# Kernel optimization log

Hardware: AMD Instinct MI355X
Metric: run time of the kernel (lower is better)

Reference implementation:

```python
import jax, jax.numpy as jnp
import numpy as np
from jax import lax


def setup_inputs() -> dict:
    key = jax.random.key(0)
    ks = jax.random.split(key, 8)
    B, T, F, H = 256, 96, 32, 1024
    s = 0.05
    return {
        "initial_input": jax.random.normal(ks[0], (B, 1, F), jnp.float32),
        "hidden_h": jax.random.normal(ks[1], (B, H), jnp.float32),
        "hidden_c": jax.random.normal(ks[2], (B, H), jnp.float32),
        "targets": jax.random.normal(ks[3], (B, T, F), jnp.float32),
        "W_x": jax.random.normal(ks[4], (F, 4 * H), jnp.float32) * s,
        "W_h": jax.random.normal(ks[5], (H, 4 * H), jnp.float32) * s,
        "b": jnp.zeros((4 * H,), jnp.float32),
        "W_dense": jax.random.normal(ks[6], (H, F), jnp.float32) * s,
        "b_dense": jnp.zeros((F,), jnp.float32),
    }


def reference(initial_input, hidden_h, hidden_c, targets, W_x, W_h, b, W_dense, b_dense):
    # Inference-mode (training=False) decode: no teacher forcing, each step's
    # dense output is fed back as the next LSTM input. Keras LSTM gate order: i, f, c(g), o.
    T = targets.shape[1]

    def step(carry, _):
        h, c, x = carry  # h,c: [B,H], x: [B,F]
        z = x @ W_x + h @ W_h + b            # [B, 4H]
        i, f, g, o = jnp.split(z, 4, axis=-1)
        i = jax.nn.sigmoid(i)
        f = jax.nn.sigmoid(f)
        g = jnp.tanh(g)
        o = jax.nn.sigmoid(o)
        c_new = f * c + i * g
        h_new = o * jnp.tanh(c_new)
        y = h_new @ W_dense + b_dense        # [B, F]
        return (h_new, c_new, y), y

    x0 = initial_input[:, 0, :]              # [B, F]
    _, ys = lax.scan(step, (hidden_h, hidden_c, x0), None, length=T)
    return jnp.transpose(ys, (1, 0, 2))      # [B, T, F]
```

## Files before the change

kernel.cpp:

```cpp
#include <hip/hip_runtime.h>
#include <hip/hip_bf16.h>
#include <stdint.h>

#define B_SZ 256
#define H_SZ 1024
#define NG   4096
#define F_SZ 32
#define T_SZ 96

typedef __attribute__((ext_vector_type(8))) short short8;
typedef __attribute__((ext_vector_type(4))) float f32x4;

__device__ __forceinline__ unsigned short f2bf(float x) {
  unsigned int u = __float_as_uint(x);
  u += 0x7fffu + ((u >> 16) & 1u);
  return (unsigned short)(u >> 16);
}
__device__ __forceinline__ float sigf(float x) {
  float e = __expf(-x);
  return __builtin_amdgcn_rcpf(1.f + e);
}
__device__ __forceinline__ float tanh_fast(float x) {
  float e = __expf(-2.f * fabsf(x));
  float t = (1.f - e) * __builtin_amdgcn_rcpf(1.f + e);
  return copysignf(t, x);
}
__device__ __forceinline__ void stage16c(const void* g, void* l) {
  __builtin_amdgcn_global_load_lds(
      (const __attribute__((address_space(1))) void*)g,
      (__attribute__((address_space(3))) void*)l, 16, 0, 1 );
}
__device__ __forceinline__ short8 u4s8(uint4 v) {
  union { uint4 u; short8 s; } c; c.u = v; return c.s;
}

__global__ __launch_bounds__(256) void k_prep_w(
    const float* __restrict__ Wx, const float* __restrict__ Wh,
    const float* __restrict__ Wd,
    unsigned short* __restrict__ WeffT, unsigned short* __restrict__ WhT,
    unsigned short* __restrict__ WdT, unsigned int* __restrict__ flags)
{
  int tid = threadIdx.x;
  if (blockIdx.x == 512) {
    for (int i = 0; i < 33; ++i) flags[i * 256 + tid] = 0u;
    for (int i = 0; i < 128; ++i) {
      int idx = i * 256 + tid;
      int f = idx >> 10, k = idx & 1023;
      WdT[idx] = f2bf(Wd[k * 32 + f]);
    }
    return;
  }
  __shared__ float wx[32 * 256];
  __shared__ unsigned short resE[32 * 256];
  __shared__ unsigned short resH[32 * 256];
  int kt = blockIdx.x & 31, nt = blockIdx.x >> 5;
  int k0 = kt * 32, n0 = nt * 256;
  for (int i = 0; i < 32; ++i) {
    int lin = i * 256 + tid;
    wx[lin] = Wx[(size_t)(lin >> 8) * NG + n0 + (lin & 255)];
  }
  __syncthreads();
  for (int kr = 0; kr < 32; ++kr) {
    int k = k0 + kr;
    float v = Wh[(size_t)k * NG + n0 + tid];
    float acc = 0.f;
#pragma unroll
    for (int f = 0; f < 32; ++f) acc += Wd[k * 32 + f] * wx[f * 256 + tid];
    resH[kr * 256 + tid] = f2bf(v);
    resE[kr * 256 + tid] = f2bf(v + acc);
  }
  __syncthreads();
#pragma unroll
  for (int pass = 0; pass < 2; ++pass) {
    const unsigned short* res = pass ? resH : resE;
    unsigned short* dst = (pass ? WhT : WeffT) + (size_t)(n0 + tid) * H_SZ + k0;
    unsigned int vals[16];
#pragma unroll
    for (int p = 0; p < 16; ++p)
      vals[p] = (unsigned int)res[(2 * p) * 256 + tid] |
                ((unsigned int)res[(2 * p + 1) * 256 + tid] << 16);
#pragma unroll
    for (int qd = 0; qd < 4; ++qd) {
      uint4 v4; v4.x = vals[4*qd]; v4.y = vals[4*qd+1]; v4.z = vals[4*qd+2]; v4.w = vals[4*qd+3];
      ((uint4*)dst)[qd] = v4;
    }
  }
}

__global__ __launch_bounds__(512, 2) void k_persist(
    const unsigned short* __restrict__ WeffT,
    const unsigned short* __restrict__ WhT,
    const float* __restrict__ x0,
    const float* __restrict__ h0,
    const float* __restrict__ c0,
    const float* __restrict__ Wx,
    const float* __restrict__ bvec,
    const float* __restrict__ bd,
    const unsigned short* __restrict__ WdT,
    unsigned short* __restrict__ hbuf0,
    unsigned short* __restrict__ hbuf1,
    float* __restrict__ out,
    unsigned int* __restrict__ flags)
{
  const int b = blockIdx.x;
  const int xcd = b & 7, slot = b >> 3;
  const int m0A = xcd << 5;
  const int m0B = m0A + 16;
  const int nh = slot << 5;
  const int tid = threadIdx.x, lane = tid & 63, w = tid >> 6;
  const int g = w >> 1;
  const int nhh = (w & 1) << 4;

  __shared__ unsigned short AbA[32 * 512];
  __shared__ unsigned short AbB[32 * 512];
  __shared__ float zldsA[4][16][33];
  __shared__ float zldsB[4][16][33];
  __shared__ float ypA[16][32];
  __shared__ float ypB[16][32];

  unsigned int* xcctab = flags + 8192;
  unsigned int myxcc;
  asm volatile("s_getreg_b32 %0, hwreg(HW_REG_XCC_ID)" : "=s"(myxcc));
  myxcc &= 15u;

  float cregA, cregB;
  {
    int m = tid >> 5, cc = tid & 31;
    size_t giA = (size_t)(m0A + m) * H_SZ + nh + cc;
    size_t giB = (size_t)(m0B + m) * H_SZ + nh + cc;
    hbuf0[giA] = f2bf(h0[giA]);
    hbuf0[giB] = f2bf(h0[giB]);
    cregA = c0[giA];
    cregB = c0[giB];
  }
  __syncthreads();
  unsigned int* myflagA = flags + (((xcd << 5) | slot) << 4);
  unsigned int* myflagB = myflagA + 4096;
  if (tid == 0) {
    __hip_atomic_store(&xcctab[b], myxcc, __ATOMIC_RELAXED,
                       __HIP_MEMORY_SCOPE_AGENT);
    __hip_atomic_store(myflagA, 1u, __ATOMIC_RELEASE, __HIP_MEMORY_SCOPE_AGENT);
    __hip_atomic_store(myflagB, 1u, __ATOMIC_RELEASE, __HIP_MEMORY_SCOPE_AGENT);
  }

  const int col = lane & 15;
  const int kq = lane >> 4;
  const int n0a = (g << 10) + nh + nhh + col;
  float bfv = bvec[n0a];
  float u0rA[4], u0rB[4];
#pragma unroll
  for (int e = 0; e < 4; ++e) { u0rA[e] = bfv; u0rB[e] = bfv; }
  for (int f = 0; f < 32; ++f) {
    float wxf = Wx[(size_t)f * NG + n0a];
    bfv += bd[f] * wxf;
#pragma unroll
    for (int e = 0; e < 4; ++e) {
      int row = (kq << 2) + e;
      u0rA[e] += x0[(m0A + row) * 32 + f] * wxf;
      u0rB[e] += x0[(m0B + row) * 32 + f] * wxf;
    }
  }

  uint4 wr[32];
  {
    const unsigned short* p0 = WhT + (size_t)n0a * H_SZ + (kq << 3);
#pragma unroll
    for (int kk = 0; kk < 32; ++kk) wr[kk] = *(const uint4*)(p0 + kk * 32);
#pragma unroll
    for (int kk = 0; kk < 32; ++kk)
      asm volatile("" : "+v"(wr[kk].x), "+v"(wr[kk].y),
                        "+v"(wr[kk].z), "+v"(wr[kk].w));
  }

  const int srow = lane >> 2;
  const int skg  = (lane & 3) ^ ((lane >> 3) & 3);
  const int sgbase = srow * H_SZ + (w << 5) + (skg << 3);
  const int q = kq ^ ((col >> 1) & 3);
  const int aoff = col * 32 + (q << 3);
  const int yf = tid & 31, ykc = tid >> 5;
  const int yrow = slot & 15;
  const int ysw = (slot >> 1) & 3;
  const bool yIsA = (slot < 16);
  const unsigned short* wdp = WdT + (size_t)yf * H_SZ + ykc * 64;
  const unsigned int* pollpA = flags + (((xcd << 5) | (lane & 31)) << 4);
  const unsigned int* pollpB = pollpA + 4096;

  bool pure = false;
  for (int j = 0; j <= T_SZ; ++j) {
    const unsigned int tgt = (unsigned)(j + 1);
    while (true) {
      unsigned int v = __hip_atomic_load(pollpA, __ATOMIC_RELAXED,
                                         __HIP_MEMORY_SCOPE_AGENT);
      if (__all(v >= tgt)) break;
      __builtin_amdgcn_s_sleep(1);
    }
    if (j == 0) {
      __builtin_amdgcn_fence(__ATOMIC_ACQUIRE, "agent");
      bool eq = (__hip_atomic_load(&xcctab[((lane & 31) << 3) | xcd],
                                   __ATOMIC_RELAXED,
                                   __HIP_MEMORY_SCOPE_AGENT) == myxcc);
      pure = __all(eq);
    } else if (!pure) {
      __builtin_amdgcn_fence(__ATOMIC_ACQUIRE, "agent");
    }
    const unsigned short* hp = (j & 1) ? hbuf1 : hbuf0;
    unsigned short* hn = (j & 1) ? hbuf0 : hbuf1;

    {
      const unsigned short* src = hp + (size_t)m0A * H_SZ + sgbase;
#pragma unroll
      for (int it = 0; it < 4; ++it)
        stage16c(src + it * 256, &AbA[it * 4096 + (w << 9)]);
      __syncthreads();
    }

    while (true) {
      unsigned int v = __hip_atomic_load(pollpB, __ATOMIC_RELAXED,
                                         __HIP_MEMORY_SCOPE_AGENT);
      if (__all(v >= tgt)) break;
      __builtin_amdgcn_s_sleep(1);
    }
    if (!pure && j > 0)
      __builtin_amdgcn_fence(__ATOMIC_ACQUIRE, "agent");
    {
      const unsigned short* src = hp + (size_t)m0B * H_SZ + sgbase;
#pragma unroll
      for (int it = 0; it < 4; ++it)
        stage16c(src + it * 256, &AbB[it * 4096 + (w << 9)]);
    }

    if (j >= 1 && yIsA) {
      float acc = 0.f;
#pragma unroll
      for (int c2 = 0; c2 < 2; ++c2) {
        const unsigned short* ab = AbA + (ykc * 2 + c2) * 512 + yrow * 32;
#pragma unroll
        for (int p = 0; p < 4; ++p) {
          uint4 av = *(const uint4*)(ab + (p << 3));
          uint4 wv = *(const uint4*)(wdp + c2 * 32 + ((p ^ ysw) << 3));
          acc += __uint_as_float(av.x << 16) * __uint_as_float(wv.x << 16);
          acc += __uint_as_float(av.x & 0xffff0000u) * __uint_as_float(wv.x & 0xffff0000u);
          acc += __uint_as_float(av.y << 16) * __uint_as_float(wv.y << 16);
          acc += __uint_as_float(av.y & 0xffff0000u) * __uint_as_float(wv.y & 0xffff0000u);
          acc += __uint_as_float(av.z << 16) * __uint_as_float(wv.z << 16);
          acc += __uint_as_float(av.z & 0xffff0000u) * __uint_as_float(wv.z & 0xffff0000u);
          acc += __uint_as_float(av.w << 16) * __uint_as_float(wv.w << 16);
          acc += __uint_as_float(av.w & 0xffff0000u) * __uint_as_float(wv.w & 0xffff0000u);
        }
      }
      ypA[ykc][yf] = acc;
    }

    if (j < T_SZ) {
      f32x4 accE, accO;
#pragma unroll
      for (int e = 0; e < 4; ++e) {
        accE[e] = (j == 0) ? u0rA[e] : bfv;
        accO[e] = 0.f;
      }
#pragma unroll
      for (int kk = 0; kk < 32; kk += 2) {
        short8 a0 = *(const short8*)(AbA + kk * 512 + aoff);
        short8 a1 = *(const short8*)(AbA + (kk + 1) * 512 + aoff);
        accE = __builtin_amdgcn_mfma_f32_16x16x32_bf16(a0, u4s8(wr[kk]), accE, 0, 0, 0);
        accO = __builtin_amdgcn_mfma_f32_16x16x32_bf16(a1, u4s8(wr[kk + 1]), accO, 0, 0, 0);
      }
#pragma unroll
      for (int e = 0; e < 4; ++e)
        zldsA[g][(kq << 2) + e][nhh + col] = accE[e] + accO[e];
    }
    __syncthreads();

    if (j < T_SZ) {
      int m = tid >> 5, cc = tid & 31;
      float zi = zldsA[0][m][cc], zf = zldsA[1][m][cc];
      float zg = zldsA[2][m][cc], zo = zldsA[3][m][cc];
      float iv = sigf(zi), fv = sigf(zf), gv = tanh_fast(zg), ov = sigf(zo);
      float cn = fv * cregA + iv * gv;
      cregA = cn;
      hn[(size_t)(m0A + m) * H_SZ + nh + cc] = f2bf(ov * tanh_fast(cn));
    }
    if (j >= 1 && yIsA && tid < 32) {
      float s = bd[tid];
#pragma unroll
      for (int kc = 0; kc < 16; ++kc) s += ypA[kc][tid];
      out[(size_t)(m0A + yrow) * (T_SZ * F_SZ) + (size_t)(j - 1) * F_SZ + tid] = s;
    }
    __syncthreads();
    if (tid == 0 && j < T_SZ) {
      if (pure)
        __hip_atomic_store(myflagA, tgt + 1, __ATOMIC_RELAXED,
                           __HIP_MEMORY_SCOPE_AGENT);
      else
        __hip_atomic_store(myflagA, tgt + 1, __ATOMIC_RELEASE,
                           __HIP_MEMORY_SCOPE_AGENT);
    }

    if (j >= 1 && !yIsA) {
      float acc = 0.f;
#pragma unroll
      for (int c2 = 0; c2 < 2; ++c2) {
        const unsigned short* ab = AbB + (ykc * 2 + c2) * 512 + yrow * 32;
#pragma unroll
        for (int p = 0; p < 4; ++p) {
          uint4 av = *(const uint4*)(ab + (p << 3));
          uint4 wv = *(const uint4*)(wdp + c2 * 32 + ((p ^ ysw) << 3));
          acc += __uint_as_float(av.x << 16) * __uint_as_float(wv.x << 16);
          acc += __uint_as_float(av.x & 0xffff0000u) * __uint_as_float(wv.x & 0xffff0000u);
          acc += __uint_as_float(av.y << 16) * __uint_as_float(wv.y << 16);
          acc += __uint_as_float(av.y & 0xffff0000u) * __uint_as_float(wv.y & 0xffff0000u);
          acc += __uint_as_float(av.z << 16) * __uint_as_float(wv.z << 16);
          acc += __uint_as_float(av.z & 0xffff0000u) * __uint_as_float(wv.z & 0xffff0000u);
          acc += __uint_as_float(av.w << 16) * __uint_as_float(wv.w << 16);
          acc += __uint_as_float(av.w & 0xffff0000u) * __uint_as_float(wv.w & 0xffff0000u);
        }
      }
      ypB[ykc][yf] = acc;
    }

    if (j < T_SZ) {
      f32x4 accE, accO;
#pragma unroll
      for (int e = 0; e < 4; ++e) {
        accE[e] = (j == 0) ? u0rB[e] : bfv;
        accO[e] = 0.f;
      }
#pragma unroll
      for (int kk = 0; kk < 32; kk += 2) {
        short8 a0 = *(const short8*)(AbB + kk * 512 + aoff);
        short8 a1 = *(const short8*)(AbB + (kk + 1) * 512 + aoff);
        accE = __builtin_amdgcn_mfma_f32_16x16x32_bf16(a0, u4s8(wr[kk]), accE, 0, 0, 0);
        accO = __builtin_amdgcn_mfma_f32_16x16x32_bf16(a1, u4s8(wr[kk + 1]), accO, 0, 0, 0);
      }
      if (j == 0) {
        const unsigned short* p0 = WeffT + (size_t)n0a * H_SZ + (kq << 3);
#pragma unroll
        for (int kk = 0; kk < 32; ++kk) wr[kk] = *(const uint4*)(p0 + kk * 32);
#pragma unroll
        for (int kk = 0; kk < 32; ++kk)
          asm volatile("" : "+v"(wr[kk].x), "+v"(wr[kk].y),
                            "+v"(wr[kk].z), "+v"(wr[kk].w));
      }
#pragma unroll
      for (int e = 0; e < 4; ++e)
        zldsB[g][(kq << 2) + e][nhh + col] = accE[e] + accO[e];
    }
    __syncthreads();

    if (j < T_SZ) {
      int m = tid >> 5, cc = tid & 31;
      float zi = zldsB[0][m][cc], zf = zldsB[1][m][cc];
      float zg = zldsB[2][m][cc], zo = zldsB[3][m][cc];
      float iv = sigf(zi), fv = sigf(zf), gv = tanh_fast(zg), ov = sigf(zo);
      float cn = fv * cregB + iv * gv;
      cregB = cn;
      hn[(size_t)(m0B + m) * H_SZ + nh + cc] = f2bf(ov * tanh_fast(cn));
    }
    if (j >= 1 && !yIsA && tid < 32) {
      float s = bd[tid];
#pragma unroll
      for (int kc = 0; kc < 16; ++kc) s += ypB[kc][tid];
      out[(size_t)(m0B + yrow) * (T_SZ * F_SZ) + (size_t)(j - 1) * F_SZ + tid] = s;
    }
    __syncthreads();
    if (tid == 0 && j < T_SZ) {
      if (pure)
        __hip_atomic_store(myflagB, tgt + 1, __ATOMIC_RELAXED,
                           __HIP_MEMORY_SCOPE_AGENT);
      else
        __hip_atomic_store(myflagB, tgt + 1, __ATOMIC_RELEASE,
                           __HIP_MEMORY_SCOPE_AGENT);
    }
  }
}

extern "C" void kernel_launch(void* const* d_in, const int* in_sizes, int n_in,
                              void* d_out, int out_size, void* d_ws, size_t ws_size,
                              hipStream_t stream)
{
  const float* x0 = (const float*)d_in[0];
  const float* h0 = (const float*)d_in[1];
  const float* c0 = (const float*)d_in[2];
  const float* Wx = (const float*)d_in[4];
  const float* Wh = (const float*)d_in[5];
  const float* bv = (const float*)d_in[6];
  const float* Wd = (const float*)d_in[7];
  const float* bd = (const float*)d_in[8];
  float* out = (float*)d_out;

  char* p = (char*)d_ws;
  unsigned short* WeffT = (unsigned short*)p; p += (size_t)NG * H_SZ * 2;
  unsigned short* WhT   = (unsigned short*)p; p += (size_t)NG * H_SZ * 2;
  unsigned short* WdT   = (unsigned short*)p; p += (size_t)F_SZ * H_SZ * 2;
  unsigned short* hb0   = (unsigned short*)p; p += (size_t)B_SZ * H_SZ * 2;
  unsigned short* hb1   = (unsigned short*)p; p += (size_t)B_SZ * H_SZ * 2;
  unsigned int* flags   = (unsigned int*)p;  p += 8704 * 4;
  (void)ws_size; (void)in_sizes; (void)n_in; (void)out_size;

  k_prep_w<<<dim3(513), dim3(256), 0, stream>>>(Wx, Wh, Wd, WeffT, WhT, WdT, flags);

  k_persist<<<dim3(256), dim3(512), 0, stream>>>(
      WeffT, WhT, x0, h0, c0, Wx, bv, bd, WdT, hb0, hb1, out, flags);
}
```

Measured before the change: 711.9 us.

## Halve persistent block to 4 waves, each owning two 16-column MFMA tiles

The persistent LSTM kernel now runs 256 threads per block instead of 512. Each wave keeps two 16-column slices of the recurrent weights in registers (64 uint4) and issues interleaved MFMAs for both. The h staging is rewritten so each wave loads 8 k-chunks with a slot-rotated order and a different swizzle, and the gate and dense-projection work is redistributed to match. The aim is fewer waves to synchronise per step and more MFMA work per A-fragment load, at the cost of doubled register pressure and less latency hiding per block.

New measurement: 749.0 us. 5.2% more time.

```diff
diff --git a/kernel.cpp b/kernel.cpp
--- a/kernel.cpp
+++ b/kernel.cpp
@@ -87,7 +87,7 @@
   }
 }
 
-__global__ __launch_bounds__(512, 2) void k_persist(
+__global__ __launch_bounds__(256, 1) void k_persist(
     const unsigned short* __restrict__ WeffT,
     const unsigned short* __restrict__ WhT,
     const float* __restrict__ x0,
@@ -107,31 +107,31 @@
   const int m0A = xcd << 5;
   const int m0B = m0A + 16;
   const int nh = slot << 5;
-  const int tid = threadIdx.x, lane = tid & 63, w = tid >> 6;
-  const int g = w >> 1;
-  const int nhh = (w & 1) << 4;
+  const int tid = threadIdx.x, lane = tid & 63, g = tid >> 6;
 
   __shared__ unsigned short AbA[32 * 512];
   __shared__ unsigned short AbB[32 * 512];
   __shared__ float zldsA[4][16][33];
   __shared__ float zldsB[4][16][33];
-  __shared__ float ypA[16][32];
-  __shared__ float ypB[16][32];
+  __shared__ float ypA[8][32];
+  __shared__ float ypB[8][32];
 
   unsigned int* xcctab = flags + 8192;
   unsigned int myxcc;
   asm volatile("s_getreg_b32 %0, hwreg(HW_REG_XCC_ID)" : "=s"(myxcc));
   myxcc &= 15u;
 
-  float cregA, cregB;
-  {
-    int m = tid >> 5, cc = tid & 31;
+  float cregA[2], cregB[2];
+#pragma unroll
+  for (int e = 0; e < 2; ++e) {
+    int idx = e * 256 + tid;
+    int m = idx >> 5, cc = idx & 31;
     size_t giA = (size_t)(m0A + m) * H_SZ + nh + cc;
     size_t giB = (size_t)(m0B + m) * H_SZ + nh + cc;
     hbuf0[giA] = f2bf(h0[giA]);
     hbuf0[giB] = f2bf(h0[giB]);
-    cregA = c0[giA];
-    cregB = c0[giB];
+    cregA[e] = c0[giA];
+    cregB[e] = c0[giB];
   }
   __syncthreads();
   unsigned int* myflagA = flags + (((xcd << 5) | slot) << 4);
@@ -145,43 +145,57 @@
 
   const int col = lane & 15;
   const int kq = lane >> 4;
-  const int n0a = (g << 10) + nh + nhh + col;
-  float bfv = bvec[n0a];
-  float u0rA[4], u0rB[4];
-#pragma unroll
-  for (int e = 0; e < 4; ++e) { u0rA[e] = bfv; u0rB[e] = bfv; }
+  const int n0c0 = (g << 10) + nh + col;
+  const int n0c1 = n0c0 + 16;
+  float bfv0 = bvec[n0c0], bfv1 = bvec[n0c1];
+  float u0rA[2][4], u0rB[2][4];
+#pragma unroll
+  for (int e = 0; e < 4; ++e) {
+    u0rA[0][e] = bfv0; u0rA[1][e] = bfv1;
+    u0rB[0][e] = bfv0; u0rB[1][e] = bfv1;
+  }
   for (int f = 0; f < 32; ++f) {
-    float wxf = Wx[(size_t)f * NG + n0a];
-    bfv += bd[f] * wxf;
+    float wx0 = Wx[(size_t)f * NG + n0c0];
+    float wx1 = Wx[(size_t)f * NG + n0c1];
+    bfv0 += bd[f] * wx0; bfv1 += bd[f] * wx1;
 #pragma unroll
     for (int e = 0; e < 4; ++e) {
       int row = (kq << 2) + e;
-      u0rA[e] += x0[(m0A + row) * 32 + f] * wxf;
-      u0rB[e] += x0[(m0B + row) * 32 + f] * wxf;
-    }
-  }
-
-  uint4 wr[32];
+      float xA = x0[(m0A + row) * 32 + f];
+      float xB = x0[(m0B + row) * 32 + f];
+      u0rA[0][e] += xA * wx0; u0rA[1][e] += xA * wx1;
+      u0rB[0][e] += xB * wx0; u0rB[1][e] += xB * wx1;
+    }
+  }
+
+  uint4 wr0[32], wr1[32];
   {
-    const unsigned short* p0 = WhT + (size_t)n0a * H_SZ + (kq << 3);
-#pragma unroll
-    for (int kk = 0; kk < 32; ++kk) wr[kk] = *(const uint4*)(p0 + kk * 32);
-#pragma unroll
-    for (int kk = 0; kk < 32; ++kk)
-      asm volatile("" : "+v"(wr[kk].x), "+v"(wr[kk].y),
-                        "+v"(wr[kk].z), "+v"(wr[kk].w));
+    const unsigned short* p0 = WhT + (size_t)n0c0 * H_SZ + (kq << 3);
+    const unsigned short* p1 = WhT + (size_t)n0c1 * H_SZ + (kq << 3);
+#pragma unroll
+    for (int kk = 0; kk < 32; ++kk) {
+      wr0[kk] = *(const uint4*)(p0 + kk * 32);
+      wr1[kk] = *(const uint4*)(p1 + kk * 32);
+    }
+#pragma unroll
+    for (int kk = 0; kk < 32; ++kk) {
+      asm volatile("" : "+v"(wr0[kk].x), "+v"(wr0[kk].y),
+                        "+v"(wr0[kk].z), "+v"(wr0[kk].w));
+      asm volatile("" : "+v"(wr1[kk].x), "+v"(wr1[kk].y),
+                        "+v"(wr1[kk].z), "+v"(wr1[kk].w));
+    }
   }
 
   const int srow = lane >> 2;
-  const int skg  = (lane & 3) ^ ((lane >> 3) & 3);
-  const int sgbase = srow * H_SZ + (w << 5) + (skg << 3);
+  const int skg  = (lane & 3) ^ ((srow >> 1) & 3);
+  const int sgoff = srow * H_SZ + (skg << 3);
   const int q = kq ^ ((col >> 1) & 3);
   const int aoff = col * 32 + (q << 3);
   const int yf = tid & 31, ykc = tid >> 5;
   const int yrow = slot & 15;
   const int ysw = (slot >> 1) & 3;
   const bool yIsA = (slot < 16);
-  const unsigned short* wdp = WdT + (size_t)yf * H_SZ + ykc * 64;
+  const unsigned short* wdp = WdT + (size_t)yf * H_SZ + ykc * 128;
   const unsigned int* pollpA = flags + (((xcd << 5) | (lane & 31)) << 4);
   const unsigned int* pollpB = pollpA + 4096;
 
@@ -207,10 +221,12 @@
     unsigned short* hn = (j & 1) ? hbuf0 : hbuf1;
 
     {
-      const unsigned short* src = hp + (size_t)m0A * H_SZ + sgbase;
-#pragma unroll
-      for (int it = 0; it < 4; ++it)
-        stage16c(src + it * 256, &AbA[it * 4096 + (w << 9)]);
+      const unsigned short* srcb = hp + (size_t)m0A * H_SZ + sgoff;
+#pragma unroll
+      for (int it = 0; it < 8; ++it) {
+        int c = (g + it * 4 + slot) & 31;
+        stage16c(srcb + c * 32, &AbA[c * 512]);
+      }
       __syncthreads();
     }
 
@@ -223,17 +239,19 @@
     if (!pure && j > 0)
       __builtin_amdgcn_fence(__ATOMIC_ACQUIRE, "agent");
     {
-      const unsigned short* src = hp + (size_t)m0B * H_SZ + sgbase;
-#pragma unroll
-      for (int it = 0; it < 4; ++it)
-        stage16c(src + it * 256, &AbB[it * 4096 + (w << 9)]);
+      const unsigned short* srcb = hp + (size_t)m0B * H_SZ + sgoff;
+#pragma unroll
+      for (int it = 0; it < 8; ++it) {
+        int c = (g + it * 4 + slot) & 31;
+        stage16c(srcb + c * 32, &AbB[c * 512]);
+      }
     }
 
     if (j >= 1 && yIsA) {
       float acc = 0.f;
 #pragma unroll
-      for (int c2 = 0; c2 < 2; ++c2) {
-        const unsigned short* ab = AbA + (ykc * 2 + c2) * 512 + yrow * 32;
+      for (int c2 = 0; c2 < 4; ++c2) {
+        const unsigned short* ab = AbA + (ykc * 4 + c2) * 512 + yrow * 32;
 #pragma unroll
         for (int p = 0; p < 4; ++p) {
           uint4 av = *(const uint4*)(ab + (p << 3));
@@ -252,38 +270,47 @@
     }
 
     if (j < T_SZ) {
-      f32x4 accE, accO;
+      f32x4 c0E, c0O, c1E, c1O;
 #pragma unroll
       for (int e = 0; e < 4; ++e) {
-        accE[e] = (j == 0) ? u0rA[e] : bfv;
-        accO[e] = 0.f;
+        c0E[e] = (j == 0) ? u0rA[0][e] : bfv0;
+        c1E[e] = (j == 0) ? u0rA[1][e] : bfv1;
+        c0O[e] = 0.f; c1O[e] = 0.f;
       }
 #pragma unroll
       for (int kk = 0; kk < 32; kk += 2) {
         short8 a0 = *(const short8*)(AbA + kk * 512 + aoff);
         short8 a1 = *(const short8*)(AbA + (kk + 1) * 512 + aoff);
-        accE = __builtin_amdgcn_mfma_f32_16x16x32_bf16(a0, u4s8(wr[kk]), accE, 0, 0, 0);
-        accO = __builtin_amdgcn_mfma_f32_16x16x32_bf16(a1, u4s8(wr[kk + 1]), accO, 0, 0, 0);
-      }
-#pragma unroll
-      for (int e = 0; e < 4; ++e)
-        zldsA[g][(kq << 2) + e][nhh + col] = accE[e] + accO[e];
+        c0E = __builtin_amdgcn_mfma_f32_16x16x32_bf16(a0, u4s8(wr0[kk]), c0E, 0, 0, 0);
+        c1E = __builtin_amdgcn_mfma_f32_16x16x32_bf16(a0, u4s8(wr1[kk]), c1E, 0, 0, 0);
+        c0O = __builtin_amdgcn_mfma_f32_16x16x32_bf16(a1, u4s8(wr0[kk + 1]), c0O, 0, 0, 0);
+        c1O = __builtin_amdgcn_mfma_f32_16x16x32_bf16(a1, u4s8(wr1[kk + 1]), c1O, 0, 0, 0);
+      }
+#pragma unroll
+      for (int e = 0; e < 4; ++e) {
+        zldsA[g][(kq << 2) + e][col] = c0E[e] + c0O[e];
+        zldsA[g][(kq << 2) + e][16 + col] = c1E[e] + c1O[e];
+      }
     }
     __syncthreads();
 
     if (j < T_SZ) {
-      int m = tid >> 5, cc = tid & 31;
-      float zi = zldsA[0][m][cc], zf = zldsA[1][m][cc];
-      float zg = zldsA[2][m][cc], zo = zldsA[3][m][cc];
-      float iv = sigf(zi), fv = sigf(zf), gv = tanh_fast(zg), ov = sigf(zo);
-      float cn = fv * cregA + iv * gv;
-      cregA = cn;
-      hn[(size_t)(m0A + m) * H_SZ + nh + cc] = f2bf(ov * tanh_fast(cn));
+#pragma unroll
+      for (int e = 0; e < 2; ++e) {
+        int idx = e * 256 + tid;
+        int m = idx >> 5, cc = idx & 31;
+        float zi = zldsA[0][m][cc], zf = zldsA[1][m][cc];
+        float zg = zldsA[2][m][cc], zo = zldsA[3][m][cc];
+        float iv = sigf(zi), fv = sigf(zf), gv = tanh_fast(zg), ov = sigf(zo);
+        float cn = fv * cregA[e] + iv * gv;
+        cregA[e] = cn;
+        hn[(size_t)(m0A + m) * H_SZ + nh + cc] = f2bf(ov * tanh_fast(cn));
+      }
     }
     if (j >= 1 && yIsA && tid < 32) {
       float s = bd[tid];
 #pragma unroll
-      for (int kc = 0; kc < 16; ++kc) s += ypA[kc][tid];
+      for (int kc = 0; kc < 8; ++kc) s += ypA[kc][tid];
       out[(size_t)(m0A + yrow) * (T_SZ * F_SZ) + (size_t)(j - 1) * F_SZ + tid] = s;
     }
     __syncthreads();
@@ -299,8 +326,8 @@
     if (j >= 1 && !yIsA) {
       float acc = 0.f;
 #pragma unroll
-      for (int c2 = 0; c2 < 2; ++c2) {
-        const unsigned short* ab = AbB + (ykc * 2 + c2) * 512 + yrow * 32;
+      for (int c2 = 0; c2 < 4; ++c2) {
+        const unsigned short* ab = AbB + (ykc * 4 + c2) * 512 + yrow * 32;
 #pragma unroll
         for (int p = 0; p < 4; ++p) {
           uint4 av = *(const uint4*)(ab + (p << 3));
@@ -319,47 +346,63 @@
     }
 
     if (j < T_SZ) {
-      f32x4 accE, accO;
+      f32x4 c0E, c0O, c1E, c1O;
 #pragma unroll
       for (int e = 0; e < 4; ++e) {
-        accE[e] = (j == 0) ? u0rB[e] : bfv;
-        accO[e] = 0.f;
+        c0E[e] = (j == 0) ? u0rB[0][e] : bfv0;
+        c1E[e] = (j == 0) ? u0rB[1][e] : bfv1;
+        c0O[e] = 0.f; c1O[e] = 0.f;
       }
 #pragma unroll
       for (int kk = 0; kk < 32; kk += 2) {
         short8 a0 = *(const short8*)(AbB + kk * 512 + aoff);
         short8 a1 = *(const short8*)(AbB + (kk + 1) * 512 + aoff);
-        accE = __builtin_amdgcn_mfma_f32_16x16x32_bf16(a0, u4s8(wr[kk]), accE, 0, 0, 0);
-        accO = __builtin_amdgcn_mfma_f32_16x16x32_bf16(a1, u4s8(wr[kk + 1]), accO, 0, 0, 0);
+        c0E = __builtin_amdgcn_mfma_f32_16x16x32_bf16(a0, u4s8(wr0[kk]), c0E, 0, 0, 0);
+        c1E = __builtin_amdgcn_mfma_f32_16x16x32_bf16(a0, u4s8(wr1[kk]), c1E, 0, 0, 0);
+        c0O = __builtin_amdgcn_mfma_f32_16x16x32_bf16(a1, u4s8(wr0[kk + 1]), c0O, 0, 0, 0);
+        c1O = __builtin_amdgcn_mfma_f32_16x16x32_bf16(a1, u4s8(wr1[kk + 1]), c1O, 0, 0, 0);
       }
       if (j == 0) {
-        const unsigned short* p0 = WeffT + (size_t)n0a * H_SZ + (kq << 3);
-#pragma unroll
-        for (int kk = 0; kk < 32; ++kk) wr[kk] = *(const uint4*)(p0 + kk * 32);
-#pragma unroll
-        for (int kk = 0; kk < 32; ++kk)
-          asm volatile("" : "+v"(wr[kk].x), "+v"(wr[kk].y),
-                            "+v"(wr[kk].z), "+v"(wr[kk].w));
-      }
-#pragma unroll
-      for (int e = 0; e < 4; ++e)
-        zldsB[g][(kq << 2) + e][nhh + col] = accE[e] + accO[e];
+        const unsigned short* p0 = WeffT + (size_t)n0c0 * H_SZ + (kq << 3);
+        const unsigned short* p1 = WeffT + (size_t)n0c1 * H_SZ + (kq << 3);
+#pragma unroll
+        for (int kk = 0; kk < 32; ++kk) {
+          wr0[kk] = *(const uint4*)(p0 + kk * 32);
+          wr1[kk] = *(const uint4*)(p1 + kk * 32);
+        }
+#pragma unroll
+        for (int kk = 0; kk < 32; ++kk) {
+          asm volatile("" : "+v"(wr0[kk].x), "+v"(wr0[kk].y),
+                            "+v"(wr0[kk].z), "+v"(wr0[kk].w));
+          asm volatile("" : "+v"(wr1[kk].x), "+v"(wr1[kk].y),
+                            "+v"(wr1[kk].z), "+v"(wr1[kk].w));
+        }
+      }
+#pragma unroll
+      for (int e = 0; e < 4; ++e) {
+        zldsB[g][(kq << 2) + e][col] = c0E[e] + c0O[e];
+        zldsB[g][(kq << 2) + e][16 + col] = c1E[e] + c1O[e];
+      }
     }
     __syncthreads();
 
     if (j < T_SZ) {
-      int m = tid >> 5, cc = tid & 31;
-      float zi = zldsB[0][m][cc], zf = zldsB[1][m][cc];
-      float zg = zldsB[2][m][cc], zo = zldsB[3][m][cc];
-      float iv = sigf(zi), fv = sigf(zf), gv = tanh_fast(zg), ov = sigf(zo);
-      float cn = fv * cregB + iv * gv;
-      cregB = cn;
-      hn[(size_t)(m0B + m) * H_SZ + nh + cc] = f2bf(ov * tanh_fast(cn));
+#pragma unroll
+      for (int e = 0; e < 2; ++e) {
+        int idx = e * 256 + tid;
+        int m = idx >> 5, cc = idx & 31;
+        float zi = zldsB[0][m][cc], zf = zldsB[1][m][cc];
+        float zg = zldsB[2][m][cc], zo = zldsB[3][m][cc];
+        float iv = sigf(zi), fv = sigf(zf), gv = tanh_fast(zg), ov = sigf(zo);
+        float cn = fv * cregB[e] + iv * gv;
+        cregB[e] = cn;
+        hn[(size_t)(m0B + m) * H_SZ + nh + cc] = f2bf(ov * tanh_fast(cn));
+      }
     }
     if (j >= 1 && !yIsA && tid < 32) {
       float s = bd[tid];
 #pragma unroll
-      for (int kc = 0; kc < 16; ++kc) s += ypB[kc][tid];
+      for (int kc = 0; kc < 8; ++kc) s += ypB[kc][tid];
       out[(size_t)(m0B + yrow) * (T_SZ * F_SZ) + (size_t)(j - 1) * F_SZ + tid] = s;
     }
     __syncthreads();
@@ -399,6 +442,6 @@
 
   k_prep_w<<<dim3(513), dim3(256), 0, stream>>>(Wx, Wh, Wd, WeffT, WhT, WdT, flags);
 
-  k_persist<<<dim3(256), dim3(512), 0, stream>>>(
+  k_persist<<<dim3(256), dim3(256), 0, stream>>>(
       WeffT, WhT, x0, h0, c0, Wx, bv, bd, WdT, hb0, hb1, out, flags);
 }
```

## Replace all-to-all flag polling with per-XCD leader that publishes an epoch

Applied to the files above, without the earlier changes.

Each block used to poll all 32 peer arrival flags in its XCD group at every step, for both the A and B halves. Now only slot 0's first wave polls the 32 flags and then writes a per-XCD epoch word, which all other blocks spin on. This is meant to cut atomic polling traffic on shared cache lines from 32x32 readers down to one. The cost is an extra hop of latency through the leader block, plus more flag memory to zero. The epoch store is relaxed, so ordering relies on the later acquire fence in the impure case.

Result: slower. 824.0 us (+15.7%).

```diff
diff --git a/kernel.cpp b/kernel.cpp
--- a/kernel.cpp
+++ b/kernel.cpp
@@ -42,7 +42,7 @@
 {
   int tid = threadIdx.x;
   if (blockIdx.x == 512) {
-    for (int i = 0; i < 33; ++i) flags[i * 256 + tid] = 0u;
+    for (int i = 0; i < 34; ++i) flags[i * 256 + tid] = 0u;
     for (int i = 0; i < 128; ++i) {
       int idx = i * 256 + tid;
       int f = idx >> 10, k = idx & 1023;
@@ -118,7 +118,9 @@
   __shared__ float ypA[16][32];
   __shared__ float ypB[16][32];
 
-  unsigned int* xcctab = flags + 8192;
+  unsigned int* xcctab = flags + 8448;
+  unsigned int* epochA = flags + 8192 + (xcd << 4);
+  unsigned int* epochB = flags + 8320 + (xcd << 4);
   unsigned int myxcc;
   asm volatile("s_getreg_b32 %0, hwreg(HW_REG_XCC_ID)" : "=s"(myxcc));
   myxcc &= 15u;
@@ -134,13 +136,13 @@
     cregB = c0[giB];
   }
   __syncthreads();
-  unsigned int* myflagA = flags + (((xcd << 5) | slot) << 4);
-  unsigned int* myflagB = myflagA + 4096;
+  unsigned int* arrA = flags + (((xcd << 5) | slot) << 4);
+  unsigned int* arrB = arrA + 4096;
   if (tid == 0) {
     __hip_atomic_store(&xcctab[b], myxcc, __ATOMIC_RELAXED,
                        __HIP_MEMORY_SCOPE_AGENT);
-    __hip_atomic_store(myflagA, 1u, __ATOMIC_RELEASE, __HIP_MEMORY_SCOPE_AGENT);
-    __hip_atomic_store(myflagB, 1u, __ATOMIC_RELEASE, __HIP_MEMORY_SCOPE_AGENT);
+    __hip_atomic_store(arrA, 1u, __ATOMIC_RELEASE, __HIP_MEMORY_SCOPE_AGENT);
+    __hip_atomic_store(arrB, 1u, __ATOMIC_RELEASE, __HIP_MEMORY_SCOPE_AGENT);
   }
 
   const int col = lane & 15;
@@ -182,18 +184,25 @@
   const int ysw = (slot >> 1) & 3;
   const bool yIsA = (slot < 16);
   const unsigned short* wdp = WdT + (size_t)yf * H_SZ + ykc * 64;
-  const unsigned int* pollpA = flags + (((xcd << 5) | (lane & 31)) << 4);
-  const unsigned int* pollpB = pollpA + 4096;
 
   bool pure = false;
   for (int j = 0; j <= T_SZ; ++j) {
     const unsigned int tgt = (unsigned)(j + 1);
-    while (true) {
-      unsigned int v = __hip_atomic_load(pollpA, __ATOMIC_RELAXED,
-                                         __HIP_MEMORY_SCOPE_AGENT);
-      if (__all(v >= tgt)) break;
-      __builtin_amdgcn_s_sleep(1);
-    }
+    if (slot == 0 && w == 0) {
+      const unsigned int* ap = flags + (((xcd << 5) | (lane & 31)) << 4);
+      while (true) {
+        unsigned int v = __hip_atomic_load(ap, __ATOMIC_RELAXED,
+                                           __HIP_MEMORY_SCOPE_AGENT);
+        if (__all(v >= tgt)) break;
+        __builtin_amdgcn_s_sleep(1);
+      }
+      if (lane == 0)
+        __hip_atomic_store(epochA, tgt, __ATOMIC_RELAXED,
+                           __HIP_MEMORY_SCOPE_AGENT);
+    }
+    while (__hip_atomic_load(epochA, __ATOMIC_RELAXED,
+                             __HIP_MEMORY_SCOPE_AGENT) < tgt)
+      __builtin_amdgcn_s_sleep(2);
     if (j == 0) {
       __builtin_amdgcn_fence(__ATOMIC_ACQUIRE, "agent");
       bool eq = (__hip_atomic_load(&xcctab[((lane & 31) << 3) | xcd],
@@ -214,12 +223,21 @@
       __syncthreads();
     }
 
-    while (true) {
-      unsigned int v = __hip_atomic_load(pollpB, __ATOMIC_RELAXED,
-                                         __HIP_MEMORY_SCOPE_AGENT);
-      if (__all(v >= tgt)) break;
-      __builtin_amdgcn_s_sleep(1);
-    }
+    if (slot == 0 && w == 0) {
+      const unsigned int* bp = flags + 4096 + (((xcd << 5) | (lane & 31)) << 4);
+      while (true) {
+        unsigned int v = __hip_atomic_load(bp, __ATOMIC_RELAXED,
+                                           __HIP_MEMORY_SCOPE_AGENT);
+        if (__all(v >= tgt)) break;
+        __builtin_amdgcn_s_sleep(1);
+      }
+      if (lane == 0)
+        __hip_atomic_store(epochB, tgt, __ATOMIC_RELAXED,
+                           __HIP_MEMORY_SCOPE_AGENT);
+    }
+    while (__hip_atomic_load(epochB, __ATOMIC_RELAXED,
+                             __HIP_MEMORY_SCOPE_AGENT) < tgt)
+      __builtin_amdgcn_s_sleep(2);
     if (!pure && j > 0)
       __builtin_amdgcn_fence(__ATOMIC_ACQUIRE, "agent");
     {
@@ -289,10 +307,10 @@
     __syncthreads();
     if (tid == 0 && j < T_SZ) {
       if (pure)
-        __hip_atomic_store(myflagA, tgt + 1, __ATOMIC_RELAXED,
+        __hip_atomic_store(arrA, tgt + 1, __ATOMIC_RELAXED,
                            __HIP_MEMORY_SCOPE_AGENT);
       else
-        __hip_atomic_store(myflagA, tgt + 1, __ATOMIC_RELEASE,
+        __hip_atomic_store(arrA, tgt + 1, __ATOMIC_RELEASE,
                            __HIP_MEMORY_SCOPE_AGENT);
     }
 
@@ -365,10 +383,10 @@
     __syncthreads();
     if (tid == 0 && j < T_SZ) {
       if (pure)
-        __hip_atomic_store(myflagB, tgt + 1, __ATOMIC_RELAXED,
+        __hip_atomic_store(arrB, tgt + 1, __ATOMIC_RELAXED,
                            __HIP_MEMORY_SCOPE_AGENT);
       else
-        __hip_atomic_store(myflagB, tgt + 1, __ATOMIC_RELEASE,
+        __hip_atomic_store(arrB, tgt + 1, __ATOMIC_RELEASE,
                            __HIP_MEMORY_SCOPE_AGENT);
     }
   }
```
